# Performance work log

Hardware: AMD Instinct MI355X
Metric: run time of the kernel (lower is better)

The kernel has to match this reference:

```python
import jax, jax.numpy as jnp
import numpy as np

HEADS = 12
DIM_HEAD = 64
PATCHES = 196  # tokens_to_attend (space attention)
DIM = 768
BATCH = 8
FRAMES = 16
TOKENS = FRAMES * PATCHES + 1  # + CLS


def setup_inputs() -> dict:
    key = jax.random.key(0)
    k1, k2, k3 = jax.random.split(key, 3)
    x = jax.random.normal(k1, (BATCH, TOKENS, DIM), dtype=jnp.float32)
    # small init scale keeps softmax logits in a sane range
    W_qkv = jax.random.normal(k2, (DIM, 3 * HEADS * DIM_HEAD), dtype=jnp.float32) * 0.02
    W_0 = jax.random.normal(k3, (HEADS * DIM_HEAD, DIM), dtype=jnp.float32) * 0.02
    return {"x": x, "W_qkv": W_qkv, "W_0": W_0}


def _mhsa(q, k, v, scale):
    # q: [g,h,i,d], k/v: [g,h,j,d]
    s = jnp.einsum('ghid,ghjd->ghij', q, k) * scale
    a = jax.nn.softmax(s, axis=-1)
    return jnp.einsum('ghij,ghjd->ghid', a, v)


def reference(x, W_qkv, W_0):
    b, t, _ = x.shape
    h, dh, p = HEADS, DIM_HEAD, PATCHES
    scale = dh ** -0.5

    qkv = x @ W_qkv  # [b,t,dh*3*h], flattened in (d, k, h) order per einops pattern
    qkv = qkv.reshape(b, t, dh, 3, h)
    q = jnp.transpose(qkv[:, :, :, 0, :], (0, 3, 1, 2))  # [b,h,t,d]
    k = jnp.transpose(qkv[:, :, :, 1, :], (0, 3, 1, 2))
    v = jnp.transpose(qkv[:, :, :, 2, :], (0, 3, 1, 2))

    # CLS query attends over ALL space-time tokens
    cls_q, q3 = q[:, :, :1], q[:, :, 1:]
    out_cls = _mhsa(cls_q, k, v, scale)  # [b,h,1,d]

    cls_k, k3 = k[:, :, :1], k[:, :, 1:]
    cls_v, v3 = v[:, :, :1], v[:, :, 1:]

    f = (t - 1) // p  # frames

    def space_rearrange(z):  # 'b h (f p) d -> (b f) h p d'
        z = z.reshape(b, h, f, p, dh)
        return jnp.transpose(z, (0, 2, 1, 3, 4)).reshape(b * f, h, p, dh)

    q_sep = space_rearrange(q3)
    k_sep = space_rearrange(k3)
    v_sep = space_rearrange(v3)

    # broadcast CLS key/value to every frame group: 'b ... -> (b tile) ...'
    cls_k = jnp.repeat(cls_k, f, axis=0)  # [b*f,h,1,d]
    cls_v = jnp.repeat(cls_v, f, axis=0)

    kk = jnp.concatenate((cls_k, k_sep), axis=2)  # [b*f,h,p+1,d]
    vv = jnp.concatenate((cls_v, v_sep), axis=2)

    out_sp = _mhsa(q_sep, kk, vv, scale)  # [b*f,h,p,d]

    # merge: '(b f) h p d -> b h (f p) d' (space=True path)
    out_sp = out_sp.reshape(b, f, h, p, dh)
    out_sp = jnp.transpose(out_sp, (0, 2, 1, 3, 4)).reshape(b, h, f * p, dh)

    out = jnp.concatenate((out_cls, out_sp), axis=2)  # [b,h,t,d]
    out = jnp.transpose(out, (0, 2, 1, 3)).reshape(b, t, h * dh)
    return out @ W_0
```

## Files before the change

### kernel.cpp

```cpp
#include <hip/hip_runtime.h>
#include <hip/hip_bf16.h>
#include <cstdint>

typedef unsigned short u16;
typedef uint32_t u32;
typedef __attribute__((ext_vector_type(8))) u16 u16x8;
typedef __attribute__((ext_vector_type(4))) u16 u16x4;
typedef __attribute__((ext_vector_type(8))) __bf16 bf16x8;
typedef __attribute__((ext_vector_type(4))) float f32x4;

#define B_    8
#define T_    3137
#define H_    12
#define F_    16
#define D_    768
#define M1    25096
#define VSTR  3200
#define NSPL  8
#define SPK   400

__device__ __forceinline__ u16 f2bf(float f) {
  unsigned u = __float_as_uint(f);
  return (u16)((u + 0x7FFFu + ((u >> 16) & 1u)) >> 16);
}
__device__ __forceinline__ float b2f(u16 v) {
  return __uint_as_float(((unsigned)v) << 16);
}

#define GLL(g, l) __builtin_amdgcn_global_load_lds( \
    (const __attribute__((address_space(1))) void*)(g), \
    (__attribute__((address_space(3))) void*)(l), 16, 0, 0)

__device__ __forceinline__ void dsr(bf16x8& d, u32 abyte) {
  asm volatile("ds_read_b128 %0, %1" : "=v"(d) : "v"(abyte));
}

__global__ __launch_bounds__(256) void k_cvt_x(const float* __restrict__ x,
                                               u16* __restrict__ xb, int n4) {
  int i = blockIdx.x * 256 + threadIdx.x;
  if (i >= n4) return;
  float4 v = ((const float4*)x)[i];
  u16x4 o = { f2bf(v.x), f2bf(v.y), f2bf(v.z), f2bf(v.w) };
  *(u16x4*)(xb + (size_t)i * 4) = o;
}

__global__ __launch_bounds__(256) void k_transpose(const float* __restrict__ in,
                                                   u16* __restrict__ out,
                                                   int R, int C, int qkvperm) {
  __shared__ float tile[32][33];
  int c0 = blockIdx.x * 32, r0 = blockIdx.y * 32;
  int tx = threadIdx.x, ty = threadIdx.y;
  #pragma unroll
  for (int i = ty; i < 32; i += 8)
    tile[i][tx] = in[(size_t)(r0 + i) * C + c0 + tx];
  __syncthreads();
  #pragma unroll
  for (int i = ty; i < 32; i += 8) {
    int c = c0 + i;
    int orow;
    if (qkvperm) {
      int d = c / 36, rem = c - d * 36;
      int comp = rem / 12, hh = rem - comp * 12;
      orow = comp * 768 + hh * 64 + d;
    } else {
      orow = c;
    }
    out[(size_t)orow * R + r0 + tx] = f2bf(tile[tx][i]);
  }
}

template<int EPI, int NX>
__global__ __launch_bounds__(256, 2) void k_gemm(const u16* __restrict__ A,
                                                 const u16* __restrict__ Bm,
                                                 float* __restrict__ outF,
                                                 u16* __restrict__ Qb,
                                                 u16* __restrict__ Kb,
                                                 u16* __restrict__ Vt) {
  __shared__ u16 lds[32768];
  const int tid = threadIdx.x;
  const int lane = tid & 63;
  const int wid = tid >> 6;
  const int wr = wid >> 1, wc = wid & 1;
  const int li = lane & 15, lg = lane >> 4;

  const int nwg = NX * 197;
  const int q = nwg >> 3, r = nwg & 7;
  const int g = blockIdx.x;
  const int xcd = g & 7, pos = g >> 3;
  const int s = ((xcd < r) ? xcd * (q + 1) : r * (q + 1) + (xcd - r) * q) + pos;
  const int arow0 = (s / NX) * 128;
  const int brow0 = (s % NX) * 128;

  const int srow = wid * 32 + (lane >> 3);
  const int scol = ((lane & 7) ^ (lane >> 3)) * 8;
  const u16* gA = A  + (size_t)(arow0 + srow) * 768 + scol;
  const u16* gB = Bm + (size_t)(brow0 + srow) * 768 + scol;

  const u32 ldsb = (u32)(uintptr_t)(__attribute__((address_space(3))) u16*)(&lds[0]);
  const u32 e0 = (u32)((lg ^ (li & 7)) * 16);
  const u32 e1 = (u32)(((lg + 4) ^ (li & 7)) * 16);
  const u32 aA = ldsb + (u32)(wr * 64 + li) * 128;
  const u32 aB = ldsb + 16384 + (u32)(wc * 64 + li) * 128;

  f32x4 acc[4][4] = {};

#define STAGE(TB, KS) do { const int kb_ = (KS) * 64; \
    _Pragma("unroll") for (int c_ = 0; c_ < 4; ++c_) { \
      GLL(gA + kb_ + c_ * 8 * 768, lds + (TB) * 16384 + wid * 2048 + c_ * 512); \
      GLL(gB + kb_ + c_ * 8 * 768, lds + (TB) * 16384 + 8192 + wid * 2048 + c_ * 512); \
    } \
  } while (0)

#define STEP(CUR, KV) do { \
    { const int ks_ = ((KV) + 1 < 12) ? (KV) + 1 : 11; STAGE((CUR) ^ 1, ks_); } \
    asm volatile("s_waitcnt vmcnt(8)"); \
    __builtin_amdgcn_s_barrier(); \
    bf16x8 af[4][2], bfr[4][2]; \
    _Pragma("unroll") for (int m = 0; m < 4; ++m) { \
      dsr(af[m][0], aA + (CUR) * 32768 + m * 2048 + e0); \
      dsr(af[m][1], aA + (CUR) * 32768 + m * 2048 + e1); } \
    _Pragma("unroll") for (int n = 0; n < 4; ++n) { \
      dsr(bfr[n][0], aB + (CUR) * 32768 + n * 2048 + e0); \
      dsr(bfr[n][1], aB + (CUR) * 32768 + n * 2048 + e1); } \
    asm volatile("s_waitcnt lgkmcnt(0)"); \
    __builtin_amdgcn_sched_barrier(0); \
    __builtin_amdgcn_s_setprio(1); \
    _Pragma("unroll") for (int m = 0; m < 4; ++m) \
    _Pragma("unroll") for (int n = 0; n < 4; ++n) { \
      acc[m][n] = __builtin_amdgcn_mfma_f32_16x16x32_bf16(af[m][0], bfr[n][0], acc[m][n], 0, 0, 0); \
      acc[m][n] = __builtin_amdgcn_mfma_f32_16x16x32_bf16(af[m][1], bfr[n][1], acc[m][n], 0, 0, 0); } \
    __builtin_amdgcn_s_setprio(0); \
    __builtin_amdgcn_s_barrier(); \
  } while (0)

  STAGE(0, 0);

  #pragma unroll 1
  for (int kk = 0; kk < 12; kk += 2) {
    STEP(0, kk);
    STEP(1, kk + 1);
  }
#undef STAGE
#undef STEP

  if (EPI == 0) {
    #pragma unroll
    for (int m = 0; m < 4; ++m)
      #pragma unroll
      for (int n = 0; n < 4; ++n) {
        const int colp = brow0 + wc * 64 + n * 16 + li;
        #pragma unroll
        for (int rr = 0; rr < 4; ++rr) {
          const int row = arow0 + wr * 64 + m * 16 + lg * 4 + rr;
          if (row < M1) outF[(size_t)row * 768 + colp] = acc[m][n][rr];
        }
      }
  } else {
    const int comp = brow0 / 768;
    const int b0r = arow0 / T_;
    const int RB = (b0r + 1) * T_;
    __syncthreads();
    if (comp < 2) {
      u16* tl = &lds[0];
      #pragma unroll
      for (int m = 0; m < 4; ++m)
        #pragma unroll
        for (int n = 0; n < 4; ++n)
          #pragma unroll
          for (int rr = 0; rr < 4; ++rr)
            tl[(wr * 64 + m * 16 + lg * 4 + rr) * 136 + wc * 64 + n * 16 + li] =
                f2bf(acc[m][n][rr]);
      __syncthreads();
      u16* dst = (comp == 0) ? Qb : Kb;
      const int hh0 = (brow0 - comp * 768) >> 6;
      const int grp = tid >> 4, li2 = tid & 15;
      #pragma unroll
      for (int pass = 0; pass < 16; ++pass) {
        const int idx = pass * 16 + grp;
        const int row = idx >> 1, hl = idx & 1;
        const int rg = arow0 + row;
        if (rg >= M1) continue;
        const int bb = (rg >= RB) ? b0r + 1 : b0r;
        const int tt = rg - bb * T_;
        const size_t bh = (size_t)bb * H_ + hh0 + hl;
        *(u16x4*)(dst + ((bh * T_ + tt) << 6) + li2 * 4) =
            *(const u16x4*)(tl + row * 136 + hl * 64 + li2 * 4);
      }
    } else {
      u16* tl = &lds[0];
      #pragma unroll
      for (int m = 0; m < 4; ++m)
        #pragma unroll
        for (int n = 0; n < 4; ++n)
          #pragma unroll
          for (int rr = 0; rr < 4; ++rr)
            tl[(wr * 64 + m * 16 + lg * 4 + rr) * 130 + wc * 64 + n * 16 + li] =
                f2bf(acc[m][n][rr]);
      __syncthreads();
      const int vcol0 = brow0 - 1536;
      #pragma unroll 1
      for (int cc = 0; cc < 32; ++cc) {
        const int c = wid * 32 + cc;
        const int vcol = vcol0 + c;
        const int hh = vcol >> 6, dd = vcol & 63;
        #pragma unroll
        for (int half = 0; half < 2; ++half) {
          const int tloc = half * 64 + lane;
          const int rg = arow0 + tloc;
          if (rg >= M1) continue;
          const int bb = (rg >= RB) ? b0r + 1 : b0r;
          const int tt = rg - bb * T_;
          Vt[(((size_t)bb * H_ + hh) * 64 + dd) * VSTR + tt] = tl[tloc * 130 + c];
        }
      }
    }
  }
}

__global__ __launch_bounds__(512, 2) void k_attn_sp(const u16* __restrict__ Qb,
                                                    const u16* __restrict__ Kb,
                                                    const u16* __restrict__ Vt,
                                                    u16* __restrict__ AO) {
  __shared__ u16 Ks[224 * 64];
  __shared__ u16 Vs[4 * 64 * 64];
  __shared__ u16 P[8][16 * 232];
  const int bid = blockIdx.x;
  const int h = bid % H_;
  const int f = (bid / H_) % F_;
  const int b = bid / (H_ * F_);
  const int tid = threadIdx.x;
  const int lane = tid & 63, w = tid >> 6;
  const int li = lane & 15, lg = lane >> 4;
  const size_t bh = (size_t)b * H_ + h;
  const u16* Qp = Qb + bh * T_ * 64;
  const u16* Kp = Kb + bh * T_ * 64;
  const u16* Vp = Vt + bh * 64 * VSTR;
  u16* ps = &P[w][0];

  if (w < 7) {
    #pragma unroll
    for (int p = 0; p < 4; ++p) {
      const int c = (w * 4 + p) * 64 + lane;
      const int key = c >> 3, sp = lane & 7;
      const int tok = (key == 0) ? 0 : f * 196 + key;
      GLL(Kp + (size_t)tok * 64 + ((sp ^ (key & 7)) * 8), Ks + c * 8);
    }
  }
  {
    const int d = tid & 63, kg = (tid >> 6) & 3, sh = tid >> 8;
    #pragma unroll
    for (int st = 0; st < 2; ++st) {
      const int stt = sh + st * 2;
      const u16* src = Vp + (size_t)d * VSTR + f * 196 + stt * 64 + kg * 16;
      u16x4 a0 = *(const u16x4*)(src);
      u16x4 a1 = *(const u16x4*)(src + 4);
      u16x4 a2 = *(const u16x4*)(src + 8);
      u16x4 a3 = *(const u16x4*)(src + 12);
      if (stt == 0 && kg == 0) a0[0] = Vp[(size_t)d * VSTR];
      u16* row = Vs + stt * 4096 + d * 64;
      const int s0 = (kg * 2) ^ (d & 7), s1 = (kg * 2 + 1) ^ (d & 7);
      u16x8 w0 = { a0[0], a0[1], a0[2], a0[3], a1[0], a1[1], a1[2], a1[3] };
      u16x8 w1 = { a2[0], a2[1], a2[2], a2[3], a3[0], a3[1], a3[2], a3[3] };
      *(u16x8*)(row + s0 * 8) = w0;
      *(u16x8*)(row + s1 * 8) = w1;
    }
  }
  __syncthreads();

  for (int mt = w; mt < 13; mt += 8) {
    const int pp = mt * 16 + li;
    const int ppc = pp < 196 ? pp : 195;
    const size_t tq = 1 + f * 196 + ppc;
    const bf16x8 qf0 = *(const bf16x8*)(Qp + tq * 64 + lg * 8);
    const bf16x8 qf1 = *(const bf16x8*)(Qp + tq * 64 + 32 + lg * 8);

    f32x4 s[14] = {};
    #pragma unroll
    for (int n = 0; n < 14; ++n) {
      const int key = n * 16 + li;
      const u16* kp = Ks + key * 64;
      const bf16x8 kf0 = *(const bf16x8*)(kp + ((lg ^ (li & 7)) * 8));
      const bf16x8 kf1 = *(const bf16x8*)(kp + (((lg + 4) ^ (li & 7)) * 8));
      s[n] = __builtin_amdgcn_mfma_f32_16x16x32_bf16(qf0, kf0, s[n], 0, 0, 0);
      s[n] = __builtin_amdgcn_mfma_f32_16x16x32_bf16(qf1, kf1, s[n], 0, 0, 0);
    }

    float rsum[4];
    #pragma unroll
    for (int r = 0; r < 4; ++r) {
      float vals[14];
      float mx = -1e30f;
      #pragma unroll
      for (int n = 0; n < 14; ++n) {
        const int key = n * 16 + li;
        float sv = s[n][r] * 0.125f;
        vals[n] = (key < 197) ? sv : -1e30f;
        mx = fmaxf(mx, vals[n]);
      }
      #pragma unroll
      for (int msk = 1; msk < 16; msk <<= 1) mx = fmaxf(mx, __shfl_xor(mx, msk));
      float sum = 0.f;
      #pragma unroll
      for (int n = 0; n < 14; ++n) {
        const int key = n * 16 + li;
        float p = (key < 197) ? __expf(vals[n] - mx) : 0.f;
        sum += p;
        ps[(lg * 4 + r) * 232 + key] = f2bf(p);
      }
      #pragma unroll
      for (int msk = 1; msk < 16; msk <<= 1) sum += __shfl_xor(sum, msk);
      rsum[r] = sum;
    }

    f32x4 o[4] = {};
    #pragma unroll
    for (int ks = 0; ks < 7; ++ks) {
      const bf16x8 pf = *(const bf16x8*)(ps + li * 232 + ks * 32 + lg * 8);
      const int slot = ((ks & 1) * 4 + lg);
      #pragma unroll
      for (int n = 0; n < 4; ++n) {
        const int d = n * 16 + li;
        const bf16x8 vf = *(const bf16x8*)(Vs + (ks >> 1) * 4096 + d * 64 +
                                           ((slot ^ (li & 7)) * 8));
        o[n] = __builtin_amdgcn_mfma_f32_16x16x32_bf16(pf, vf, o[n], 0, 0, 0);
      }
    }

    #pragma unroll
    for (int n = 0; n < 4; ++n) {
      const int d = n * 16 + li;
      #pragma unroll
      for (int r = 0; r < 4; ++r) {
        const int ppo = mt * 16 + lg * 4 + r;
        if (ppo < 196) {
          const size_t t = 1 + (size_t)f * 196 + ppo;
          AO[((size_t)b * T_ + t) * 768 + h * 64 + d] = f2bf(o[n][r] / rsum[r]);
        }
      }
    }
  }
}

__global__ __launch_bounds__(256) void k_attn_cls1(const u16* __restrict__ Qb,
                                                   const u16* __restrict__ Kb,
                                                   const u16* __restrict__ Vt,
                                                   float* __restrict__ Pc) {
  __shared__ float qs[64];
  __shared__ float sv[SPK];
  __shared__ float red[8];
  const int bid = blockIdx.x;
  const int s = bid & (NSPL - 1);
  const int bh = bid >> 3;
  const u16* Qp = Qb + (size_t)bh * T_ * 64;
  const u16* Kp = Kb + (size_t)bh * T_ * 64;
  const u16* Vp = Vt + (size_t)bh * 64 * VSTR;
  const int base = s * SPK;
  const int nk = (T_ - base < SPK) ? (T_ - base) : SPK;
  const int tid = threadIdx.x;
  const int lane = tid & 63, w = tid >> 6;

  if (tid < 64) qs[tid] = b2f(Qp[tid]);
  for (int jj = nk + tid; jj < SPK; jj += 256) sv[jj] = 0.f;
  __syncthreads();

  float lmax = -1e30f;
  for (int jj = tid; jj < nk; jj += 256) {
    const u16* kp = Kp + (size_t)(base + jj) * 64;
    float acc = 0.f;
    #pragma unroll
    for (int d0 = 0; d0 < 64; d0 += 8) {
      u16x8 kv = *(const u16x8*)(kp + d0);
      #pragma unroll
      for (int e = 0; e < 8; ++e) acc += qs[d0 + e] * b2f(kv[e]);
    }
    acc *= 0.125f;
    sv[jj] = acc;
    lmax = fmaxf(lmax, acc);
  }
  #pragma unroll
  for (int msk = 32; msk; msk >>= 1) lmax = fmaxf(lmax, __shfl_xor(lmax, msk));
  if (lane == 0) red[w] = lmax;
  __syncthreads();
  const float bmax = fmaxf(fmaxf(red[0], red[1]), fmaxf(red[2], red[3]));

  float lsum = 0.f;
  for (int jj = tid; jj < nk; jj += 256) {
    float p = __expf(sv[jj] - bmax);
    sv[jj] = p;
    lsum += p;
  }
  #pragma unroll
  for (int msk = 32; msk; msk >>= 1) lsum += __shfl_xor(lsum, msk);
  if (lane == 0) red[4 + w] = lsum;
  __syncthreads();
  const float bsum = red[4] + red[5] + red[6] + red[7];

  const int d = tid >> 2, q4 = tid & 3;
  const u16* vp = Vp + (size_t)d * VSTR + base + q4 * (SPK / 4);
  const float* sp = &sv[q4 * (SPK / 4)];
  float o = 0.f;
  #pragma unroll
  for (int k4 = 0; k4 < SPK / 4; k4 += 4) {
    u16x4 vv = *(const u16x4*)(vp + k4);
    o += sp[k4]     * b2f(vv[0]) + sp[k4 + 1] * b2f(vv[1])
       + sp[k4 + 2] * b2f(vv[2]) + sp[k4 + 3] * b2f(vv[3]);
  }
  o += __shfl_xor(o, 1);
  o += __shfl_xor(o, 2);

  float* P = Pc + ((size_t)bh * NSPL + s) * 66;
  if (tid == 0) { P[0] = bmax; P[1] = bsum; }
  if (q4 == 0) P[2 + d] = o;
}

__global__ __launch_bounds__(64) void k_attn_cls2(const float* __restrict__ Pc,
                                                  u16* __restrict__ AO) {
  const int bh = blockIdx.x;
  const int d = threadIdx.x;
  const float* P = Pc + (size_t)bh * NSPL * 66;
  float m = -1e30f;
  #pragma unroll
  for (int s = 0; s < NSPL; ++s) m = fmaxf(m, P[s * 66]);
  float l = 0.f, o = 0.f;
  #pragma unroll
  for (int s = 0; s < NSPL; ++s) {
    const float wgt = __expf(P[s * 66] - m);
    l += wgt * P[s * 66 + 1];
    o += wgt * P[s * 66 + 2 + d];
  }
  const int b = bh / H_, h = bh - b * H_;
  AO[(size_t)b * T_ * 768 + h * 64 + d] = f2bf(o / l);
}

extern "C" void kernel_launch(void* const* d_in, const int* in_sizes, int n_in,
                              void* d_out, int out_size, void* d_ws, size_t ws_size,
                              hipStream_t stream) {
  const float* x    = (const float*)d_in[0];
  const float* Wqkv = (const float*)d_in[1];
  const float* W0   = (const float*)d_in[2];
  float* out = (float*)d_out;
  char* ws = (char*)d_ws;

  u16* xb    = (u16*)(ws);
  u16* wqkvT = (u16*)(ws + 38731776);
  u16* w0T   = (u16*)(ws + 42270720);
  u16* Qb    = (u16*)(ws + 43450368);
  u16* Kb    = (u16*)(ws + 81997824);
  u16* Vt    = (u16*)(ws + 120545280);
  u16* AO = xb;
  float* Pc = (float*)wqkvT;

  k_cvt_x<<<dim3(18822), dim3(256), 0, stream>>>(x, xb, (M1 * D_) / 4);
  k_transpose<<<dim3(72, 24), dim3(32, 8), 0, stream>>>(Wqkv, wqkvT, 768, 2304, 1);
  k_transpose<<<dim3(24, 24), dim3(32, 8), 0, stream>>>(W0, w0T, 768, 768, 0);
  k_gemm<1, 18><<<dim3(18 * 197), dim3(256), 0, stream>>>(xb, wqkvT, nullptr, Qb, Kb, Vt);
  k_attn_sp<<<dim3(1536), dim3(512), 0, stream>>>(Qb, Kb, Vt, AO);
  k_attn_cls1<<<dim3(96 * NSPL), dim3(256), 0, stream>>>(Qb, Kb, Vt, Pc);
  k_attn_cls2<<<dim3(96), dim3(64), 0, stream>>>(Pc, AO);
  k_gemm<0, 6><<<dim3(6 * 197), dim3(256), 0, stream>>>(AO, w0T, out, nullptr, nullptr, nullptr);
}
```

Baseline: 289.1 us.

## Use 256x256-tile 8-wave ping-pong GEMM for QKV projection with swizzled epilogue

Replaces the 128x128 QKV projection GEMM with a 512-thread kernel computing 256x256 tiles. It uses a fine-grained interleaved schedule of LDS reads, global-to-LDS prefetches and MFMA sub-blocks separated by barriers. The larger tile raises operand reuse and halves global traffic per flop. The epilogue uses an XOR-swizzled LDS staging layout and nontemporal stores, and the output GEMM also switches to nontemporal stores. The trade-offs are higher register and LDS pressure (128 KB LDS), fewer workgroups (891) that may leave tail imbalance, and more barriers.

```diff
diff --git a/kernel.cpp b/kernel.cpp
--- a/kernel.cpp
+++ b/kernel.cpp
@@ -27,6 +27,10 @@
   return __uint_as_float(((unsigned)v) << 16);
 }
 
+__device__ __forceinline__ int swz(int row, int col) {
+  return row * 256 + (((col >> 3) ^ (row & 7)) << 3) + (col & 7);
+}
+
 #define GLL(g, l) __builtin_amdgcn_global_load_lds( \
     (const __attribute__((address_space(1))) void*)(g), \
     (__attribute__((address_space(3))) void*)(l), 16, 0, 0)
@@ -34,6 +38,14 @@
 __device__ __forceinline__ void dsr(bf16x8& d, u32 abyte) {
   asm volatile("ds_read_b128 %0, %1" : "=v"(d) : "v"(abyte));
 }
+
+#define BARR  __builtin_amdgcn_s_barrier()
+#define LGKM0 asm volatile("s_waitcnt lgkmcnt(0)")
+#define VMC4  asm volatile("s_waitcnt vmcnt(4)")
+#define VMC0  asm volatile("s_waitcnt vmcnt(0)")
+#define SCB   __builtin_amdgcn_sched_barrier(0)
+#define PRI1  __builtin_amdgcn_s_setprio(1)
+#define PRI0  __builtin_amdgcn_s_setprio(0)
 
 __global__ __launch_bounds__(256) void k_cvt_x(const float* __restrict__ x,
                                                u16* __restrict__ xb, int n4) {
@@ -69,13 +81,162 @@
   }
 }
 
-template<int EPI, int NX>
-__global__ __launch_bounds__(256, 2) void k_gemm(const u16* __restrict__ A,
-                                                 const u16* __restrict__ Bm,
-                                                 float* __restrict__ outF,
-                                                 u16* __restrict__ Qb,
-                                                 u16* __restrict__ Kb,
-                                                 u16* __restrict__ Vt) {
+__global__ __launch_bounds__(512, 2) void k_gemm8(const u16* __restrict__ A,
+                                                  const u16* __restrict__ Bm,
+                                                  u16* __restrict__ Qb,
+                                                  u16* __restrict__ Kb,
+                                                  u16* __restrict__ Vt) {
+  __shared__ u16 lds[65536];
+  const int tid = threadIdx.x;
+  const int lane = tid & 63, wid = tid >> 6;
+  const int wr = wid >> 2, wc = wid & 3;
+  const int li = lane & 15, lg = lane >> 4;
+
+  const int nwg = 891, q = nwg >> 3, r = nwg & 7;
+  const int g = blockIdx.x;
+  const int xcd = g & 7, pos = g >> 3;
+  const int s = ((xcd < r) ? xcd * (q + 1) : r * (q + 1) + (xcd - r) * q) + pos;
+  const int arow0 = (s / 9) * 256;
+  const int brow0 = (s % 9) * 256;
+
+  const int rl = wid * 8 + (lane >> 3);
+  const int sl = ((lane & 7) ^ (lane >> 3)) * 8;
+  u32 oA[2][2], oB[2][2];
+  #pragma unroll
+  for (int hh = 0; hh < 2; ++hh)
+    #pragma unroll
+    for (int j = 0; j < 2; ++j) {
+      const int grow = hh * 128 + j * 64 + rl;
+      int ra = arow0 + grow; if (ra >= M1) ra = M1 - 1;
+      oA[hh][j] = (u32)ra * 768u + sl;
+      oB[hh][j] = (u32)(brow0 + grow) * 768u + sl;
+    }
+
+  const u32 ldsb = (u32)(uintptr_t)(__attribute__((address_space(3))) u16*)(&lds[0]);
+  const u32 e0 = (u32)((lg ^ (li & 7)) * 16);
+  const u32 e1 = (u32)(((lg + 4) ^ (li & 7)) * 16);
+  const u32 aA = ldsb + (u32)wr * 16384 + (u32)li * 128;
+  const u32 aB = ldsb + 32768 + (u32)(wc >> 1) * 16384 + (u32)((wc & 1) * 64 + li) * 128;
+
+  f32x4 acc[8][4] = {};
+  bf16x8 af[4][2], af2[4][2], bf0[2][2], bf1[2][2];
+
+#define STA(bufU, hh, kt) do { \
+    GLL(A + oA[hh][0] + (kt), lds + (bufU) + (hh) * 8192 + wid * 512); \
+    GLL(A + oA[hh][1] + (kt), lds + (bufU) + (hh) * 8192 + wid * 512 + 4096); } while (0)
+#define STB(bufU, hh, kt) do { \
+    GLL(Bm + oB[hh][0] + (kt), lds + (bufU) + 16384 + (hh) * 8192 + wid * 512); \
+    GLL(Bm + oB[hh][1] + (kt), lds + (bufU) + 16384 + (hh) * 8192 + wid * 512 + 4096); } while (0)
+#define RDA(dst, curB, mofs) do { _Pragma("unroll") for (int mf_ = 0; mf_ < 4; ++mf_) { \
+    dsr(dst[mf_][0], aA + (curB) + (mofs) + mf_ * 2048 + e0); \
+    dsr(dst[mf_][1], aA + (curB) + (mofs) + mf_ * 2048 + e1); } } while (0)
+#define RDB(dst, curB, nofs) do { _Pragma("unroll") for (int nf_ = 0; nf_ < 2; ++nf_) { \
+    dsr(dst[nf_][0], aB + (curB) + (nofs) + nf_ * 2048 + e0); \
+    dsr(dst[nf_][1], aB + (curB) + (nofs) + nf_ * 2048 + e1); } } while (0)
+#define MM(AF, BF, MB, NB) do { \
+    _Pragma("unroll") for (int mf_ = 0; mf_ < 4; ++mf_) \
+    _Pragma("unroll") for (int nf_ = 0; nf_ < 2; ++nf_) \
+    _Pragma("unroll") for (int kk_ = 0; kk_ < 2; ++kk_) \
+      acc[(MB) + mf_][(NB) + nf_] = __builtin_amdgcn_mfma_f32_16x16x32_bf16( \
+        AF[mf_][kk_], BF[nf_][kk_], acc[(MB) + mf_][(NB) + nf_], 0, 0, 0); } while (0)
+
+  STA(0, 0, 0); STA(0, 1, 0); STB(0, 0, 0); STB(0, 1, 0);
+  STA(32768, 0, 64); STA(32768, 1, 64);
+  VMC4; BARR;
+
+  #pragma unroll 1
+  for (int it = 0; it < 6; ++it) {
+    const int k1 = (2 * it + 1) * 64;
+    const int k2 = ((2 * it + 2 < 12) ? 2 * it + 2 : 11) * 64;
+    const int k3 = ((2 * it + 3 < 12) ? 2 * it + 3 : 11) * 64;
+    RDA(af, 0, 0); RDB(bf0, 0, 0); STB(32768, 0, k1);
+    BARR; LGKM0; SCB; PRI1; MM(af, bf0, 0, 0); PRI0; BARR;
+    RDA(af2, 0, 8192); STB(32768, 1, k1);
+    BARR; LGKM0; SCB; PRI1; MM(af2, bf0, 4, 0); PRI0; BARR;
+    RDB(bf1, 0, 4096); STA(0, 0, k2);
+    BARR; LGKM0; SCB; PRI1; MM(af, bf1, 0, 2); PRI0; BARR;
+    STA(0, 1, k2); VMC4;
+    BARR; SCB; PRI1; MM(af2, bf1, 4, 2); PRI0; BARR;
+    RDA(af, 65536, 0); RDB(bf0, 65536, 0); STB(0, 0, k2);
+    BARR; LGKM0; SCB; PRI1; MM(af, bf0, 0, 0); PRI0; BARR;
+    RDA(af2, 65536, 8192); STB(0, 1, k2);
+    BARR; LGKM0; SCB; PRI1; MM(af2, bf0, 4, 0); PRI0; BARR;
+    RDB(bf1, 65536, 4096); STA(32768, 0, k3);
+    BARR; LGKM0; SCB; PRI1; MM(af, bf1, 0, 2); PRI0; BARR;
+    STA(32768, 1, k3); VMC4;
+    BARR; SCB; PRI1; MM(af2, bf1, 4, 2); PRI0; BARR;
+  }
+#undef STA
+#undef STB
+#undef RDA
+#undef RDB
+#undef MM
+
+  VMC0;
+  __syncthreads();
+  const int comp = brow0 / 768;
+  const int b0r = arow0 / T_;
+  const int RB = (b0r + 1) * T_;
+  if (comp < 2) {
+    u16* tl = &lds[0];
+    #pragma unroll
+    for (int mf = 0; mf < 8; ++mf)
+      #pragma unroll
+      for (int nf = 0; nf < 4; ++nf)
+        #pragma unroll
+        for (int rr = 0; rr < 4; ++rr)
+          tl[swz(wr * 128 + mf * 16 + lg * 4 + rr, wc * 64 + nf * 16 + li)] =
+              f2bf(acc[mf][nf][rr]);
+    __syncthreads();
+    u16* dst = comp ? Kb : Qb;
+    const int hh0 = (brow0 - comp * 768) >> 6;
+    const int grp = tid >> 4, li2 = tid & 15;
+    #pragma unroll
+    for (int pass = 0; pass < 32; ++pass) {
+      const int idx = pass * 32 + grp;
+      const int row = idx >> 2, hl = idx & 3;
+      const int rg = arow0 + row;
+      if (rg >= M1) continue;
+      const int bb = (rg >= RB) ? b0r + 1 : b0r;
+      const int tt = rg - bb * T_;
+      const size_t bh = (size_t)bb * H_ + hh0 + hl;
+      u16x4 v = *(const u16x4*)(tl + swz(row, hl * 64 + li2 * 4));
+      __builtin_nontemporal_store(v, (u16x4*)(dst + ((bh * T_ + tt) << 6) + li2 * 4));
+    }
+  } else {
+    u16* tl = &lds[0];
+    #pragma unroll
+    for (int mf = 0; mf < 8; ++mf)
+      #pragma unroll
+      for (int nf = 0; nf < 4; ++nf)
+        #pragma unroll
+        for (int rr = 0; rr < 4; ++rr)
+          tl[swz(wr * 128 + mf * 16 + lg * 4 + rr, wc * 64 + nf * 16 + li)] =
+              f2bf(acc[mf][nf][rr]);
+    __syncthreads();
+    const int vcol0 = brow0 - 1536;
+    #pragma unroll 1
+    for (int cc = 0; cc < 32; ++cc) {
+      const int c = wid * 32 + cc;
+      const int vcol = vcol0 + c;
+      const int hh = vcol >> 6, dd = vcol & 63;
+      #pragma unroll
+      for (int qt = 0; qt < 4; ++qt) {
+        const int tloc = qt * 64 + lane;
+        const int rg = arow0 + tloc;
+        if (rg >= M1) continue;
+        const int bb = (rg >= RB) ? b0r + 1 : b0r;
+        const int tt = rg - bb * T_;
+        __builtin_nontemporal_store(tl[swz(tloc, c)],
+            Vt + (((size_t)bb * H_ + hh) * 64 + dd) * VSTR + tt);
+      }
+    }
+  }
+}
+
+__global__ __launch_bounds__(256, 2) void k_gemmB(const u16* __restrict__ A,
+                                                  const u16* __restrict__ Bm,
+                                                  float* __restrict__ outF) {
   __shared__ u16 lds[32768];
   const int tid = threadIdx.x;
   const int lane = tid & 63;
@@ -83,13 +244,13 @@
   const int wr = wid >> 1, wc = wid & 1;
   const int li = lane & 15, lg = lane >> 4;
 
-  const int nwg = NX * 197;
+  const int nwg = 6 * 197;
   const int q = nwg >> 3, r = nwg & 7;
   const int g = blockIdx.x;
   const int xcd = g & 7, pos = g >> 3;
   const int s = ((xcd < r) ? xcd * (q + 1) : r * (q + 1) + (xcd - r) * q) + pos;
-  const int arow0 = (s / NX) * 128;
-  const int brow0 = (s % NX) * 128;
+  const int arow0 = (s / 6) * 128;
+  const int brow0 = (s % 6) * 128;
 
   const int srow = wid * 32 + (lane >> 3);
   const int scol = ((lane & 7) ^ (lane >> 3)) * 8;
@@ -114,7 +275,7 @@
 #define STEP(CUR, KV) do { \
     { const int ks_ = ((KV) + 1 < 12) ? (KV) + 1 : 11; STAGE((CUR) ^ 1, ks_); } \
     asm volatile("s_waitcnt vmcnt(8)"); \
-    __builtin_amdgcn_s_barrier(); \
+    BARR; \
     bf16x8 af[4][2], bfr[4][2]; \
     _Pragma("unroll") for (int m = 0; m < 4; ++m) { \
       dsr(af[m][0], aA + (CUR) * 32768 + m * 2048 + e0); \
@@ -122,15 +283,12 @@
     _Pragma("unroll") for (int n = 0; n < 4; ++n) { \
       dsr(bfr[n][0], aB + (CUR) * 32768 + n * 2048 + e0); \
       dsr(bfr[n][1], aB + (CUR) * 32768 + n * 2048 + e1); } \
-    asm volatile("s_waitcnt lgkmcnt(0)"); \
-    __builtin_amdgcn_sched_barrier(0); \
-    __builtin_amdgcn_s_setprio(1); \
+    LGKM0; SCB; PRI1; \
     _Pragma("unroll") for (int m = 0; m < 4; ++m) \
     _Pragma("unroll") for (int n = 0; n < 4; ++n) { \
       acc[m][n] = __builtin_amdgcn_mfma_f32_16x16x32_bf16(af[m][0], bfr[n][0], acc[m][n], 0, 0, 0); \
       acc[m][n] = __builtin_amdgcn_mfma_f32_16x16x32_bf16(af[m][1], bfr[n][1], acc[m][n], 0, 0, 0); } \
-    __builtin_amdgcn_s_setprio(0); \
-    __builtin_amdgcn_s_barrier(); \
+    PRI0; BARR; \
   } while (0)
 
   STAGE(0, 0);
@@ -143,78 +301,18 @@
 #undef STAGE
 #undef STEP
 
-  if (EPI == 0) {
-    #pragma unroll
-    for (int m = 0; m < 4; ++m)
-      #pragma unroll
-      for (int n = 0; n < 4; ++n) {
-        const int colp = brow0 + wc * 64 + n * 16 + li;
-        #pragma unroll
-        for (int rr = 0; rr < 4; ++rr) {
-          const int row = arow0 + wr * 64 + m * 16 + lg * 4 + rr;
-          if (row < M1) outF[(size_t)row * 768 + colp] = acc[m][n][rr];
-        }
+  #pragma unroll
+  for (int m = 0; m < 4; ++m)
+    #pragma unroll
+    for (int n = 0; n < 4; ++n) {
+      const int colp = brow0 + wc * 64 + n * 16 + li;
+      #pragma unroll
+      for (int rr = 0; rr < 4; ++rr) {
+        const int row = arow0 + wr * 64 + m * 16 + lg * 4 + rr;
+        if (row < M1)
+          __builtin_nontemporal_store(acc[m][n][rr], outF + (size_t)row * 768 + colp);
       }
-  } else {
-    const int comp = brow0 / 768;
-    const int b0r = arow0 / T_;
-    const int RB = (b0r + 1) * T_;
-    __syncthreads();
-    if (comp < 2) {
-      u16* tl = &lds[0];
-      #pragma unroll
-      for (int m = 0; m < 4; ++m)
-        #pragma unroll
-        for (int n = 0; n < 4; ++n)
-          #pragma unroll
-          for (int rr = 0; rr < 4; ++rr)
-            tl[(wr * 64 + m * 16 + lg * 4 + rr) * 136 + wc * 64 + n * 16 + li] =
-                f2bf(acc[m][n][rr]);
-      __syncthreads();
-      u16* dst = (comp == 0) ? Qb : Kb;
-      const int hh0 = (brow0 - comp * 768) >> 6;
-      const int grp = tid >> 4, li2 = tid & 15;
-      #pragma unroll
-      for (int pass = 0; pass < 16; ++pass) {
-        const int idx = pass * 16 + grp;
-        const int row = idx >> 1, hl = idx & 1;
-        const int rg = arow0 + row;
-        if (rg >= M1) continue;
-        const int bb = (rg >= RB) ? b0r + 1 : b0r;
-        const int tt = rg - bb * T_;
-        const size_t bh = (size_t)bb * H_ + hh0 + hl;
-        *(u16x4*)(dst + ((bh * T_ + tt) << 6) + li2 * 4) =
-            *(const u16x4*)(tl + row * 136 + hl * 64 + li2 * 4);
-      }
-    } else {
-      u16* tl = &lds[0];
-      #pragma unroll
-      for (int m = 0; m < 4; ++m)
-        #pragma unroll
-        for (int n = 0; n < 4; ++n)
-          #pragma unroll
-          for (int rr = 0; rr < 4; ++rr)
-            tl[(wr * 64 + m * 16 + lg * 4 + rr) * 130 + wc * 64 + n * 16 + li] =
-                f2bf(acc[m][n][rr]);
-      __syncthreads();
-      const int vcol0 = brow0 - 1536;
-      #pragma unroll 1
-      for (int cc = 0; cc < 32; ++cc) {
-        const int c = wid * 32 + cc;
-        const int vcol = vcol0 + c;
-        const int hh = vcol >> 6, dd = vcol & 63;
-        #pragma unroll
-        for (int half = 0; half < 2; ++half) {
-          const int tloc = half * 64 + lane;
-          const int rg = arow0 + tloc;
-          if (rg >= M1) continue;
-          const int bb = (rg >= RB) ? b0r + 1 : b0r;
-          const int tt = rg - bb * T_;
-          Vt[(((size_t)bb * H_ + hh) * 64 + dd) * VSTR + tt] = tl[tloc * 130 + c];
-        }
-      }
-    }
-  }
+    }
 }
 
 __global__ __launch_bounds__(512, 2) void k_attn_sp(const u16* __restrict__ Qb,
@@ -453,9 +551,9 @@
   k_cvt_x<<<dim3(18822), dim3(256), 0, stream>>>(x, xb, (M1 * D_) / 4);
   k_transpose<<<dim3(72, 24), dim3(32, 8), 0, stream>>>(Wqkv, wqkvT, 768, 2304, 1);
   k_transpose<<<dim3(24, 24), dim3(32, 8), 0, stream>>>(W0, w0T, 768, 768, 0);
-  k_gemm<1, 18><<<dim3(18 * 197), dim3(256), 0, stream>>>(xb, wqkvT, nullptr, Qb, Kb, Vt);
+  k_gemm8<<<dim3(891), dim3(512), 0, stream>>>(xb, wqkvT, Qb, Kb, Vt);
   k_attn_sp<<<dim3(1536), dim3(512), 0, stream>>>(Qb, Kb, Vt, AO);
   k_attn_cls1<<<dim3(96 * NSPL), dim3(256), 0, stream>>>(Qb, Kb, Vt, Pc);
   k_attn_cls2<<<dim3(96), dim3(64), 0, stream>>>(Pc, AO);
-  k_gemm<0, 6><<<dim3(6 * 197), dim3(256), 0, stream>>>(AO, w0T, out, nullptr, nullptr, nullptr);
-}
+  k_gemmB<<<dim3(6 * 197), dim3(256), 0, stream>>>(AO, w0T, out);
+}
```

After: 477.1 us. 1.65x slower.
